# Kernel tuning notes

Hardware: AMD Instinct MI355X
Metric: run time of the kernel (lower is better)

## Reference

```python
import jax, jax.numpy as jnp
import numpy as np


def setup_inputs() -> dict:
    key = jax.random.key(0)
    kq, kk, kv = jax.random.split(key, 3)
    B, S, D = 4, 4096, 128
    return {
        "q_proj": jax.random.normal(kq, (B, S, D), dtype=jnp.float32),
        "k_proj": jax.random.normal(kk, (B, S, D), dtype=jnp.float32),
        "v_proj": jax.random.normal(kv, (B, S, D), dtype=jnp.float32),
    }


def reference(q_proj, k_proj, v_proj):
    # Block-wise online softmax in the original is mathematically exact
    # full (non-causal) scaled dot-product attention.
    d = q_proj.shape[-1]
    scale = 1.0 / jnp.sqrt(jnp.asarray(d, dtype=q_proj.dtype))
    logits = jnp.einsum('bqd,bkd->bqk', q_proj, k_proj) * scale  # [B,S,S]
    attn = jax.nn.softmax(logits, axis=-1)
    return jnp.einsum('bqk,bkd->bqd', attn, v_proj)
```

## Files before the change

kernel.cpp:

```cpp
#include <hip/hip_runtime.h>
#include <hip/hip_bf16.h>
#include <stdint.h>

#define Bn 4
#define Sn 4096
#define Dn 128
#define SCALE 0.08838834764831843f

typedef __attribute__((ext_vector_type(8)))  short short8;
typedef __attribute__((ext_vector_type(4)))  short short4v;
typedef __attribute__((ext_vector_type(4)))  float f32x4;
typedef __attribute__((ext_vector_type(16))) float f32x16;

__device__ __forceinline__ uint32_t bfround(float f){
  union { float f; uint32_t u; } a; a.f = f;
  return a.u + 0x7FFFu + ((a.u >> 16) & 1u);
}
__device__ __forceinline__ short f2bf(float f){ return (short)(bfround(f) >> 16); }
__device__ __forceinline__ uint32_t f2bf2(float lo, float hi){
  return (bfround(hi) & 0xFFFF0000u) | (bfround(lo) >> 16);
}
__device__ __forceinline__ float bf2f(short s){
  union { uint32_t u; float f; } a; a.u = ((uint32_t)(unsigned short)s) << 16; return a.f;
}

__device__ __forceinline__ void gload16(const void* g, void* l){
  __builtin_amdgcn_global_load_lds(
      (const __attribute__((address_space(1))) unsigned int*)g,
      (__attribute__((address_space(3))) unsigned int*)l, 16, 0, 0);
}

__global__ void cvt_k_kernel(const float* __restrict__ k, short* __restrict__ kb){
  int i = blockIdx.x * blockDim.x + threadIdx.x;
  const f32x4 v = ((const f32x4*)k)[i];
  short4v s;
  s[0]=f2bf(v[0]); s[1]=f2bf(v[1]); s[2]=f2bf(v[2]); s[3]=f2bf(v[3]);
  ((short4v*)kb)[i] = s;
}

__global__ void cvt_v_kernel(const float* __restrict__ v, short* __restrict__ vt){
  __shared__ float tile[64][65];
  const int t  = threadIdx.x;
  const int s0 = blockIdx.x * 64;
  const int d0 = blockIdx.y * 64;
  const int b  = blockIdx.z;
#pragma unroll
  for (int i=0;i<16;++i){
    int lin = i*256 + t;
    int r = lin >> 6, c = lin & 63;
    tile[r][c] = v[((size_t)(b*Sn + s0 + r))*Dn + d0 + c];
  }
  __syncthreads();
#pragma unroll
  for (int i=0;i<2;++i){
    int lin = i*256 + t;
    int r = lin >> 3;
    int u = lin & 7;
    short8 s;
#pragma unroll
    for (int p=0;p<8;++p){
      int x = u*8 + p;
      int k = (x & ~15) | ((x & 3) | (((x>>2)&1)<<3) | (((x>>3)&1)<<2));
      s[p] = f2bf(tile[k][r]);
    }
    *(short8*)(vt + ((size_t)(b*Dn + d0 + r))*Sn + s0 + u*8) = s;
  }
}

__global__ __launch_bounds__(256, 2) void fa_kernel(
    const float* __restrict__ Qg, const short* __restrict__ Kb,
    const short* __restrict__ VTb, short* __restrict__ parts,
    float* __restrict__ lparts){
  __shared__ __align__(16) char lds[65536];
  const int tid = threadIdx.x;
  const int w = tid >> 6, lane = tid & 63;
  const int ln = lane & 31, h5 = lane >> 5;
  const int idx = blockIdx.x;
  const int b  = (idx >> 1) & 3;
  const int t2 = (idx & 1) | ((idx >> 3) << 1);
  const int qt = t2 >> 2, ksIdx = t2 & 3;
  const int q0 = qt * 128;
  const int k0 = ksIdx * 1024;

  short8 Qf[8];
  {
    const float* qp = Qg + ((size_t)(b*Sn + q0 + w*32 + ln))*Dn;
#pragma unroll
    for (int t=0;t<8;++t){
      const int d0 = t*16 + h5*8;
      const f32x4 a = *(const f32x4*)(qp + d0);
      const f32x4 c = *(const f32x4*)(qp + d0 + 4);
      union { uint32_t u[4]; short8 s; } pk;
      pk.u[0] = f2bf2(a[0]*SCALE, a[1]*SCALE);
      pk.u[1] = f2bf2(a[2]*SCALE, a[3]*SCALE);
      pk.u[2] = f2bf2(c[0]*SCALE, c[1]*SCALE);
      pk.u[3] = f2bf2(c[2]*SCALE, c[3]*SCALE);
      Qf[t] = pk.s;
    }
  }

  f32x16 Ot[4];
#pragma unroll
  for (int m=0;m<4;++m)
#pragma unroll
    for (int r=0;r<16;++r) Ot[m][r] = 0.0f;
  float lsum = 0.0f;

  auto stage = [&](int it, int ph){
    char* bufb = lds + ph*32768;
    if (w < 2){
#pragma unroll
      for (int u=0;u<8;++u){
        const int iu = w*8 + u;
        const int r  = iu*4 + (lane >> 4);
        const int gc = (lane & 15) ^ (r & 7);
        const char* src = (const char*)Kb + ((size_t)(b*Sn + k0 + it*64 + r))*256 + gc*16;
        gload16(src, bufb + iu*1024);
      }
    } else {
#pragma unroll
      for (int u=0;u<8;++u){
        const int iu = (w-2)*8 + u;
        const int r  = iu*8 + (lane >> 3);
        const int gc = (lane & 7) ^ (r & 7);
        const char* src = (const char*)VTb + (((size_t)(b*Dn + r))*Sn + k0 + it*64)*2 + gc*16;
        gload16(src, bufb + 16384 + iu*1024);
      }
    }
  };

  stage(0, 0);

  for (int it=0; it<16; ++it){
    const int ph = it & 1;
    __syncthreads();
    if (it < 15) stage(it+1, ph^1);

    const char* bK = lds + ph*32768;
    const char* bV = bK + 16384;

    f32x16 St0, St1;
#pragma unroll
    for (int r=0;r<16;++r){ St0[r]=0.0f; St1[r]=0.0f; }
#pragma unroll
    for (int t=0;t<8;++t){
      const int pos = ((2*t + h5) ^ (ln & 7)) * 16;
      const short8 kf0 = *(const short8*)(bK + (size_t)ln*256 + pos);
      const short8 kf1 = *(const short8*)(bK + (size_t)(32+ln)*256 + pos);
      St0 = __builtin_amdgcn_mfma_f32_32x32x16_bf16(kf0, Qf[t], St0, 0, 0, 0);
      St1 = __builtin_amdgcn_mfma_f32_32x32x16_bf16(kf1, Qf[t], St1, 0, 0, 0);
    }

    float pb[32];
#pragma unroll
    for (int r=0;r<16;++r) pb[r]    = __expf(St0[r]);
#pragma unroll
    for (int r=0;r<16;++r) pb[16+r] = __expf(St1[r]);
#pragma unroll
    for (int r=0;r<32;++r) lsum += pb[r];

    uint32_t Ppk[16];
#pragma unroll
    for (int i=0;i<16;++i) Ppk[i] = f2bf2(pb[2*i], pb[2*i+1]);

#pragma unroll
    for (int t=0;t<4;++t){
      union { uint32_t u[4]; short8 s; } pf;
      pf.u[0]=Ppk[4*t]; pf.u[1]=Ppk[4*t+1]; pf.u[2]=Ppk[4*t+2]; pf.u[3]=Ppk[4*t+3];
      const int pos = ((2*t + h5) ^ (ln & 7)) * 16;
#pragma unroll
      for (int mt=0;mt<4;++mt){
        const short8 vf = *(const short8*)(bV + (size_t)(mt*32+ln)*128 + pos);
        Ot[mt] = __builtin_amdgcn_mfma_f32_32x32x16_bf16(vf, pf.s, Ot[mt], 0, 0, 0);
      }
    }
  }

  lsum += __shfl_xor(lsum, 32, 64);

  const int slot = b*32 + qt;
  short* pbase = parts + ((size_t)(slot*4 + ksIdx))*16384 + (size_t)(w*32 + ln)*128;
#pragma unroll
  for (int mt=0;mt<4;++mt){
#pragma unroll
    for (int g=0;g<4;++g){
      union { uint32_t u[2]; short4v s; } o;
      o.u[0] = f2bf2(Ot[mt][4*g],   Ot[mt][4*g+1]);
      o.u[1] = f2bf2(Ot[mt][4*g+2], Ot[mt][4*g+3]);
      *(short4v*)(pbase + mt*32 + 8*g + 4*h5) = o.s;
    }
  }
  if (h5 == 0) lparts[(size_t)(slot*4 + ksIdx)*128 + w*32 + ln] = lsum;
}

__global__ void reduce_kernel(const short* __restrict__ parts,
                              const float* __restrict__ lparts,
                              float* __restrict__ out){
  const int t  = threadIdx.x;
  const int s  = blockIdx.x >> 3;
  const int qg = (blockIdx.x & 7)*16 + (t >> 4);
  const int d0 = (t & 15) * 8;
  float acc[8];
#pragma unroll
  for (int j=0;j<8;++j) acc[j] = 0.0f;
  float lsum = 0.0f;
#pragma unroll
  for (int ks=0;ks<4;++ks){
    const short8 p = *(const short8*)(parts + ((size_t)(s*4+ks))*16384 + (size_t)qg*128 + d0);
#pragma unroll
    for (int j=0;j<8;++j) acc[j] += bf2f(p[j]);
    lsum += lparts[(size_t)(s*4+ks)*128 + qg];
  }
  const float linv = 1.0f / lsum;
  f32x4 o0, o1;
#pragma unroll
  for (int j=0;j<4;++j){ o0[j] = acc[j]*linv; o1[j] = acc[4+j]*linv; }
  float* op = out + ((size_t)(s*128 + qg))*128 + d0;
  *(f32x4*)op = o0;
  *(f32x4*)(op + 4) = o1;
}

extern "C" void kernel_launch(void* const* d_in, const int* in_sizes, int n_in,
                              void* d_out, int out_size, void* d_ws, size_t ws_size,
                              hipStream_t stream){
  const float* q = (const float*)d_in[0];
  const float* k = (const float*)d_in[1];
  const float* v = (const float*)d_in[2];
  float* out = (float*)d_out;
  char* ws = (char*)d_ws;
  short* kb     = (short*)ws;
  short* vt     = kb + (size_t)Bn*Sn*Dn;
  short* parts  = (short*)(ws + 8388608);
  float* lparts = (float*)(ws + 8388608 + 16777216);

  cvt_k_kernel<<<(Bn*Sn*Dn/4)/256, 256, 0, stream>>>(k, kb);
  cvt_v_kernel<<<dim3(Sn/64, Dn/64, Bn), 256, 0, stream>>>(v, vt);
  fa_kernel<<<512, 256, 0, stream>>>(q, kb, vt, parts, lparts);
  reduce_kernel<<<1024, 256, 0, stream>>>(parts, lparts, out);
}
```

Measured before the change: 122.8 us.

## Merge conversion kernels, fuse split-K reduction into attention, use exp2 and cheaper bf16 packing

Folds the K and V bf16 conversion kernels into a single prep launch, and removes the separate reduce kernel. The last-arriving attention block per query tile now performs the reduction, using an atomic counter and a thread fence. Softmax folds log2(e) into the Q scale so it can use the hardware exp2. It also swaps round-to-nearest-even bf16 packing for a round-half-up add-and-permute, and splits the row sum into four accumulators. This trims launch count and ALU work, but adds atomics and a serialized tail reduction in the final blocks, plus slightly different rounding.

```diff
diff --git a/kernel.cpp b/kernel.cpp
--- a/kernel.cpp
+++ b/kernel.cpp
@@ -5,23 +5,35 @@
 #define Bn 4
 #define Sn 4096
 #define Dn 128
-#define SCALE 0.08838834764831843f
+#define SCALE ((float)(0.08838834764831843 * 1.4426950408889634))
 
 typedef __attribute__((ext_vector_type(8)))  short short8;
 typedef __attribute__((ext_vector_type(4)))  short short4v;
 typedef __attribute__((ext_vector_type(4)))  float f32x4;
 typedef __attribute__((ext_vector_type(16))) float f32x16;
+typedef __attribute__((ext_vector_type(2)))  uint32_t uint2v;
 
 __device__ __forceinline__ uint32_t bfround(float f){
   union { float f; uint32_t u; } a; a.f = f;
   return a.u + 0x7FFFu + ((a.u >> 16) & 1u);
 }
-__device__ __forceinline__ short f2bf(float f){ return (short)(bfround(f) >> 16); }
 __device__ __forceinline__ uint32_t f2bf2(float lo, float hi){
   return (bfround(hi) & 0xFFFF0000u) | (bfround(lo) >> 16);
 }
+__device__ __forceinline__ uint32_t f2bf2_fast(float lo, float hi){
+  const uint32_t a = __float_as_uint(lo) + 0x8000u;
+  const uint32_t b = __float_as_uint(hi) + 0x8000u;
+  return __builtin_amdgcn_perm(b, a, 0x07060302u);
+}
 __device__ __forceinline__ float bf2f(short s){
   union { uint32_t u; float f; } a; a.u = ((uint32_t)(unsigned short)s) << 16; return a.f;
+}
+__device__ __forceinline__ float fexp2(float x){
+#if __has_builtin(__builtin_amdgcn_exp2f)
+  return __builtin_amdgcn_exp2f(x);
+#else
+  return exp2f(x);
+#endif
 }
 
 __device__ __forceinline__ void gload16(const void* g, void* l){
@@ -30,47 +42,55 @@
       (__attribute__((address_space(3))) unsigned int*)l, 16, 0, 0);
 }
 
-__global__ void cvt_k_kernel(const float* __restrict__ k, short* __restrict__ kb){
-  int i = blockIdx.x * blockDim.x + threadIdx.x;
-  const f32x4 v = ((const f32x4*)k)[i];
-  short4v s;
-  s[0]=f2bf(v[0]); s[1]=f2bf(v[1]); s[2]=f2bf(v[2]); s[3]=f2bf(v[3]);
-  ((short4v*)kb)[i] = s;
-}
-
-__global__ void cvt_v_kernel(const float* __restrict__ v, short* __restrict__ vt){
-  __shared__ float tile[64][65];
-  const int t  = threadIdx.x;
-  const int s0 = blockIdx.x * 64;
-  const int d0 = blockIdx.y * 64;
-  const int b  = blockIdx.z;
-#pragma unroll
-  for (int i=0;i<16;++i){
-    int lin = i*256 + t;
-    int r = lin >> 6, c = lin & 63;
-    tile[r][c] = v[((size_t)(b*Sn + s0 + r))*Dn + d0 + c];
-  }
-  __syncthreads();
-#pragma unroll
-  for (int i=0;i<2;++i){
-    int lin = i*256 + t;
-    int r = lin >> 3;
-    int u = lin & 7;
-    short8 s;
-#pragma unroll
-    for (int p=0;p<8;++p){
-      int x = u*8 + p;
-      int k = (x & ~15) | ((x & 3) | (((x>>2)&1)<<3) | (((x>>3)&1)<<2));
-      s[p] = f2bf(tile[k][r]);
-    }
-    *(short8*)(vt + ((size_t)(b*Dn + d0 + r))*Sn + s0 + u*8) = s;
+__global__ void prep_kernel(const float* __restrict__ k, const float* __restrict__ v,
+                            short* __restrict__ kb, short* __restrict__ vt,
+                            int* __restrict__ ctr){
+  const int bid = blockIdx.x;
+  const int t   = threadIdx.x;
+  if (bid < 2048){
+    const int i = bid*256 + t;
+    const f32x4 val = ((const f32x4*)k)[i];
+    uint2v o;
+    o[0] = f2bf2_fast(val[0], val[1]);
+    o[1] = f2bf2_fast(val[2], val[3]);
+    *(uint2v*)(kb + 4*(size_t)i) = o;
+    if (bid == 0 && t < 128) ctr[t] = 0;
+  } else {
+    __shared__ float tile[64][65];
+    const int vb = bid - 2048;
+    const int s0 = (vb & 63) * 64;
+    const int d0 = ((vb >> 6) & 1) * 64;
+    const int b  = vb >> 7;
+#pragma unroll
+    for (int i=0;i<16;++i){
+      int lin = i*256 + t;
+      int r = lin >> 6, c = lin & 63;
+      tile[r][c] = v[((size_t)(b*Sn + s0 + r))*Dn + d0 + c];
+    }
+    __syncthreads();
+#pragma unroll
+    for (int i=0;i<2;++i){
+      int lin = i*256 + t;
+      int r = lin >> 3;
+      int u = lin & 7;
+      union { uint32_t w[4]; short8 s; } pk;
+#pragma unroll
+      for (int p=0;p<4;++p){
+        int x0 = u*8 + 2*p, x1 = x0 + 1;
+        int k0 = (x0 & ~15) | ((x0 & 3) | (((x0>>2)&1)<<3) | (((x0>>3)&1)<<2));
+        int k1 = (x1 & ~15) | ((x1 & 3) | (((x1>>2)&1)<<3) | (((x1>>3)&1)<<2));
+        pk.w[p] = f2bf2_fast(tile[k0][r], tile[k1][r]);
+      }
+      *(short8*)(vt + ((size_t)(b*Dn + d0 + r))*Sn + s0 + u*8) = pk.s;
+    }
   }
 }
 
 __global__ __launch_bounds__(256, 2) void fa_kernel(
     const float* __restrict__ Qg, const short* __restrict__ Kb,
     const short* __restrict__ VTb, short* __restrict__ parts,
-    float* __restrict__ lparts){
+    float* __restrict__ lparts, int* __restrict__ ctr,
+    float* __restrict__ Og){
   __shared__ __align__(16) char lds[65536];
   const int tid = threadIdx.x;
   const int w = tid >> 6, lane = tid & 63;
@@ -104,7 +124,7 @@
   for (int m=0;m<4;++m)
 #pragma unroll
     for (int r=0;r<16;++r) Ot[m][r] = 0.0f;
-  float lsum = 0.0f;
+  float ls0=0.f, ls1=0.f, ls2=0.f, ls3=0.f;
 
   auto stage = [&](int it, int ph){
     char* bufb = lds + ph*32768;
@@ -151,22 +171,30 @@
       St1 = __builtin_amdgcn_mfma_f32_32x32x16_bf16(kf1, Qf[t], St1, 0, 0, 0);
     }
 
-    float pb[32];
-#pragma unroll
-    for (int r=0;r<16;++r) pb[r]    = __expf(St0[r]);
-#pragma unroll
-    for (int r=0;r<16;++r) pb[16+r] = __expf(St1[r]);
-#pragma unroll
-    for (int r=0;r<32;++r) lsum += pb[r];
-
-    uint32_t Ppk[16];
-#pragma unroll
-    for (int i=0;i<16;++i) Ppk[i] = f2bf2(pb[2*i], pb[2*i+1]);
+#pragma unroll
+    for (int r=0;r<16;++r) St0[r] = fexp2(St0[r]);
+#pragma unroll
+    for (int r=0;r<16;++r) St1[r] = fexp2(St1[r]);
+#pragma unroll
+    for (int r=0;r<16;r+=4){
+      ls0 += St0[r];   ls1 += St0[r+1]; ls2 += St0[r+2]; ls3 += St0[r+3];
+      ls0 += St1[r];   ls1 += St1[r+1]; ls2 += St1[r+2]; ls3 += St1[r+3];
+    }
 
 #pragma unroll
     for (int t=0;t<4;++t){
       union { uint32_t u[4]; short8 s; } pf;
-      pf.u[0]=Ppk[4*t]; pf.u[1]=Ppk[4*t+1]; pf.u[2]=Ppk[4*t+2]; pf.u[3]=Ppk[4*t+3];
+      if (t < 2){
+        pf.u[0] = f2bf2_fast(St0[8*t+0], St0[8*t+1]);
+        pf.u[1] = f2bf2_fast(St0[8*t+2], St0[8*t+3]);
+        pf.u[2] = f2bf2_fast(St0[8*t+4], St0[8*t+5]);
+        pf.u[3] = f2bf2_fast(St0[8*t+6], St0[8*t+7]);
+      } else {
+        pf.u[0] = f2bf2_fast(St1[8*t-16], St1[8*t-15]);
+        pf.u[1] = f2bf2_fast(St1[8*t-14], St1[8*t-13]);
+        pf.u[2] = f2bf2_fast(St1[8*t-12], St1[8*t-11]);
+        pf.u[3] = f2bf2_fast(St1[8*t-10], St1[8*t-9]);
+      }
       const int pos = ((2*t + h5) ^ (ln & 7)) * 16;
 #pragma unroll
       for (int mt=0;mt<4;++mt){
@@ -176,6 +204,7 @@
     }
   }
 
+  float lsum = (ls0 + ls1) + (ls2 + ls3);
   lsum += __shfl_xor(lsum, 32, 64);
 
   const int slot = b*32 + qt;
@@ -185,39 +214,44 @@
 #pragma unroll
     for (int g=0;g<4;++g){
       union { uint32_t u[2]; short4v s; } o;
-      o.u[0] = f2bf2(Ot[mt][4*g],   Ot[mt][4*g+1]);
-      o.u[1] = f2bf2(Ot[mt][4*g+2], Ot[mt][4*g+3]);
+      o.u[0] = f2bf2_fast(Ot[mt][4*g],   Ot[mt][4*g+1]);
+      o.u[1] = f2bf2_fast(Ot[mt][4*g+2], Ot[mt][4*g+3]);
       *(short4v*)(pbase + mt*32 + 8*g + 4*h5) = o.s;
     }
   }
   if (h5 == 0) lparts[(size_t)(slot*4 + ksIdx)*128 + w*32 + ln] = lsum;
-}
-
-__global__ void reduce_kernel(const short* __restrict__ parts,
-                              const float* __restrict__ lparts,
-                              float* __restrict__ out){
-  const int t  = threadIdx.x;
-  const int s  = blockIdx.x >> 3;
-  const int qg = (blockIdx.x & 7)*16 + (t >> 4);
-  const int d0 = (t & 15) * 8;
-  float acc[8];
-#pragma unroll
-  for (int j=0;j<8;++j) acc[j] = 0.0f;
-  float lsum = 0.0f;
-#pragma unroll
-  for (int ks=0;ks<4;++ks){
-    const short8 p = *(const short8*)(parts + ((size_t)(s*4+ks))*16384 + (size_t)qg*128 + d0);
-#pragma unroll
-    for (int j=0;j<8;++j) acc[j] += bf2f(p[j]);
-    lsum += lparts[(size_t)(s*4+ks)*128 + qg];
-  }
-  const float linv = 1.0f / lsum;
-  f32x4 o0, o1;
-#pragma unroll
-  for (int j=0;j<4;++j){ o0[j] = acc[j]*linv; o1[j] = acc[4+j]*linv; }
-  float* op = out + ((size_t)(s*128 + qg))*128 + d0;
-  *(f32x4*)op = o0;
-  *(f32x4*)(op + 4) = o1;
+
+  __threadfence();
+  __syncthreads();
+  int* lastp = (int*)lds;
+  if (tid == 0) *lastp = atomicAdd(&ctr[slot], 1);
+  __syncthreads();
+  if (*lastp == 3){
+    __threadfence();
+#pragma unroll
+    for (int g=0; g<8; ++g){
+      const int q  = g*16 + (tid >> 4);
+      const int d0 = (tid & 15) * 8;
+      float acc[8];
+#pragma unroll
+      for (int j=0;j<8;++j) acc[j] = 0.0f;
+      float lq = 0.0f;
+#pragma unroll
+      for (int ks=0;ks<4;++ks){
+        const short8 p = *(const short8*)(parts + ((size_t)(slot*4+ks))*16384 + (size_t)q*128 + d0);
+#pragma unroll
+        for (int j=0;j<8;++j) acc[j] += bf2f(p[j]);
+        lq += lparts[(size_t)(slot*4+ks)*128 + q];
+      }
+      const float linv = 1.0f / lq;
+      f32x4 o0, o1;
+#pragma unroll
+      for (int j=0;j<4;++j){ o0[j] = acc[j]*linv; o1[j] = acc[4+j]*linv; }
+      float* op = Og + ((size_t)(b*Sn + q0 + q))*Dn + d0;
+      *(f32x4*)op = o0;
+      *(f32x4*)(op + 4) = o1;
+    }
+  }
 }
 
 extern "C" void kernel_launch(void* const* d_in, const int* in_sizes, int n_in,
@@ -232,9 +266,8 @@
   short* vt     = kb + (size_t)Bn*Sn*Dn;
   short* parts  = (short*)(ws + 8388608);
   float* lparts = (float*)(ws + 8388608 + 16777216);
-
-  cvt_k_kernel<<<(Bn*Sn*Dn/4)/256, 256, 0, stream>>>(k, kb);
-  cvt_v_kernel<<<dim3(Sn/64, Dn/64, Bn), 256, 0, stream>>>(v, vt);
-  fa_kernel<<<512, 256, 0, stream>>>(q, kb, vt, parts, lparts);
-  reduce_kernel<<<1024, 256, 0, stream>>>(parts, lparts, out);
-}
+  int*   ctr    = (int*)(ws + 8388608 + 16777216 + 262144);
+
+  prep_kernel<<<2560, 256, 0, stream>>>(k, v, kb, vt, ctr);
+  fa_kernel<<<512, 256, 0, stream>>>(q, kb, vt, parts, lparts, ctr, out);
+}
```

Measured after the change: 211.9 us. 72.5% more time.
